# Kernel tuning notes

Hardware: AMD Instinct MI355X
Metric: run time of the kernel (lower is better)

Reference implementation:

```python
import jax, jax.numpy as jnp
import numpy as np

DIM = 1024
AUX = 3
B, S = 32, 1024
ENC_D = DIM * AUX  # 3072


def setup_inputs() -> dict:
    key = jax.random.key(0)
    ks = jax.random.split(key, 5)
    sc1 = 1.0 / np.sqrt(DIM * (AUX + 1))
    sc3 = 1.0 / np.sqrt(ENC_D)
    return {
        "hidden_state": jax.random.normal(ks[0], (B, DIM), jnp.float32),
        "encoder_outputs": jax.random.normal(ks[1], (B, S, ENC_D), jnp.float32),
        "W1": jax.random.normal(ks[2], (DIM, DIM * (AUX + 1)), jnp.float32) * sc1,
        "b1": jnp.zeros((DIM,), jnp.float32),
        "w2": jax.random.normal(ks[3], (1, DIM), jnp.float32) * (1.0 / np.sqrt(DIM)),
        "W3": jax.random.normal(ks[4], (DIM, ENC_D), jnp.float32) * sc3,
        "b3": jnp.zeros((DIM,), jnp.float32),
    }


def reference(hidden_state, encoder_outputs, W1, b1, w2, W3, b3):
    # hidden_state: (B, dim); encoder_outputs: (B, S, dim*aux)
    Bsz, Slen, _ = encoder_outputs.shape
    h = jnp.broadcast_to(hidden_state[:, None, :], (Bsz, Slen, hidden_state.shape[-1]))
    inputs = jnp.concatenate([encoder_outputs, h], axis=2)  # (B, S, dim*(aux+1))
    # score MLP: tanh(linear1) -> linear2 (no bias)
    hidden = jnp.tanh(jnp.einsum('bsf,df->bsd', inputs, W1) + b1)  # (B, S, dim)
    e = jnp.einsum('bsd,od->bso', hidden, w2)[..., 0]  # (B, S)
    alpha = jax.nn.softmax(e, axis=1)
    context = jnp.einsum('bs,bsf->bf', alpha, encoder_outputs)  # (B, dim*aux)
    return jnp.einsum('bf,df->bd', context, W3) + b3  # (B, dim)
```

## Files before the change

### kernel.cpp

```cpp
#include <hip/hip_runtime.h>
#include <hip/hip_bf16.h>


typedef float          fx4 __attribute__((ext_vector_type(4)));
typedef short          sv8 __attribute__((ext_vector_type(8)));
typedef unsigned short uv4 __attribute__((ext_vector_type(4)));
typedef unsigned int   ui4 __attribute__((ext_vector_type(4)));

__device__ __forceinline__ unsigned short f2bf(float x) {
  unsigned u = __float_as_uint(x);
  return (unsigned short)((u + 0x7FFFu + ((u >> 16) & 1u)) >> 16);
}

__device__ __forceinline__ unsigned cvtpk(float lo, float hi) {
  unsigned r;
  asm("v_cvt_pk_bf16_f32 %0, %1, %2" : "=v"(r) : "v"(lo), "v"(hi));
  return r;
}
__device__ __forceinline__ ui4 pack8(fx4 a, fx4 b) {
  ui4 v;
  v[0] = cvtpk(a[0], a[1]); v[1] = cvtpk(a[2], a[3]);
  v[2] = cvtpk(b[0], b[1]); v[3] = cvtpk(b[2], b[3]);
  return v;
}

__global__ void convw1_kernel(const float* __restrict__ W1, unsigned short* __restrict__ W1a) {
  int id = blockIdx.x * 256 + threadIdx.x;
  int d = id / 768, fi = id - d * 768;
  fx4 v = ((const fx4*)W1)[d * 1024 + fi];
  uv4 r; r[0] = f2bf(v[0]); r[1] = f2bf(v[1]); r[2] = f2bf(v[2]); r[3] = f2bf(v[3]);
  ((uv4*)W1a)[d * 768 + fi] = r;
}

__global__ void hbias_kernel(const float* __restrict__ hs, const float* __restrict__ W1,
                             const float* __restrict__ b1, float* __restrict__ hb) {
  int idx = (blockIdx.x << 2) + (threadIdx.x >> 6);
  int lane = threadIdx.x & 63;
  int b = idx >> 10, d = idx & 1023;
  const fx4* hv = (const fx4*)hs;
  const fx4* wv = (const fx4*)W1;
  float s = 0.f;
#pragma unroll
  for (int i = 0; i < 4; ++i) {
    int k4 = lane + (i << 6);
    fx4 h = hv[(b << 8) + k4];
    fx4 w = wv[d * 1024 + 768 + k4];
    s += h[0] * w[0] + h[1] * w[1] + h[2] * w[2] + h[3] * w[3];
  }
#pragma unroll
  for (int off = 32; off; off >>= 1) s += __shfl_xor(s, off);
  if (lane == 0) hb[idx] = s + b1[d];
}

__global__ __launch_bounds__(512, 2)
void gemm_score(const float* __restrict__ enc,
                const unsigned short* __restrict__ W1a,
                const float* __restrict__ hb,
                const float* __restrict__ w2,
                float* __restrict__ pe) {
  __shared__ __align__(16) unsigned short As[2][8192];
  __shared__ __align__(16) unsigned short Bs[2][8192];

  const int t = threadIdx.x;
  const int lane = t & 63, wid = t >> 6;
  const int wm = wid >> 2, wn = wid & 3;

  const int bid = blockIdx.x;
  const int lg = ((bid & 7) << 6) | (bid >> 3);
  const int mt = lg >> 2, nt = lg & 3;
  const int row0 = mt << 8;
  const int col0 = nt << 8;

  const fx4* encv = (const fx4*)enc;

  const int ar = t >> 1, ah = t & 1;
  const int agb = (row0 + ar) * 768 + ah * 4;
  const int awb = ar * 32;
  const int ws0 = ((2 * ah + 0) ^ (ar & 3)) << 3;
  const int ws1 = ((2 * ah + 1) ^ (ar & 3)) << 3;

  const unsigned short* bsrc0 =
      W1a + (col0 + 32 * wid + (lane >> 2)) * 3072 + (((lane & 3) ^ ((lane >> 2) & 3)) << 3);
  const unsigned short* bsrc1 = bsrc0 + 16 * 3072;
  const int bdst0 = (32 * wid) * 32;
  const int bdst1 = (32 * wid + 16) * 32;

  const int r15 = lane & 15, q = lane >> 4;
  const int offA = (wm * 128 + r15) * 32 + ((q ^ (r15 & 3)) << 3);
  const int offB = (wn * 64 + r15) * 32 + ((q ^ (r15 & 3)) << 3);

  fx4 acc[8][4] = {};
  fx4 pa[4];

#define A_LOAD(kt)                                                    \
  { _Pragma("unroll")                                                 \
    for (int j = 0; j < 4; ++j) pa[j] = encv[agb + (kt) * 8 + j]; }
#define A_WRITE(bq)                                                   \
  { *(ui4*)&As[bq][awb + ws0] = pack8(pa[0], pa[1]);                  \
    *(ui4*)&As[bq][awb + ws1] = pack8(pa[2], pa[3]); }
#define B_ISSUE(bq, kt)                                               \
  { __builtin_amdgcn_global_load_lds(                                 \
        (const __attribute__((address_space(1))) void*)(bsrc0 + (kt) * 32), \
        (__attribute__((address_space(3))) void*)&Bs[bq][bdst0], 16, 0, 0); \
    __builtin_amdgcn_global_load_lds(                                 \
        (const __attribute__((address_space(1))) void*)(bsrc1 + (kt) * 32), \
        (__attribute__((address_space(3))) void*)&Bs[bq][bdst1], 16, 0, 0); }
#define COMPUTE(p)                                                    \
  { sv8 af[8], bfv[4];                                                \
    _Pragma("unroll")                                                 \
    for (int mi = 0; mi < 8; ++mi) af[mi] = *(const sv8*)&As[p][offA + mi * 512]; \
    _Pragma("unroll")                                                 \
    for (int ni = 0; ni < 4; ++ni) bfv[ni] = *(const sv8*)&Bs[p][offB + ni * 512]; \
    __builtin_amdgcn_s_setprio(1);                                    \
    _Pragma("unroll")                                                 \
    for (int mi = 0; mi < 8; ++mi)                                    \
      _Pragma("unroll")                                               \
      for (int ni = 0; ni < 4; ++ni)                                  \
        acc[mi][ni] = __builtin_amdgcn_mfma_f32_16x16x32_bf16(af[mi], bfv[ni], acc[mi][ni], 0, 0, 0); \
    __builtin_amdgcn_s_setprio(0); }
#define ITER(kt, p)                                                   \
  { COMPUTE(p)                                                        \
    if ((kt) < 95) { A_WRITE(p ^ 1) }                                 \
    if ((kt) < 94) { A_LOAD((kt) + 2) }                               \
    asm volatile("s_waitcnt lgkmcnt(0)" ::: "memory");                \
    __builtin_amdgcn_s_barrier();                                     \
    __builtin_amdgcn_sched_barrier(0);                                \
    if ((kt) < 94) {                                                  \
      B_ISSUE(p, (kt) + 2)                                            \
      asm volatile("s_waitcnt vmcnt(6)" ::: "memory");                \
    } else if ((kt) == 94) {                                          \
      asm volatile("s_waitcnt vmcnt(0)" ::: "memory");                \
    }                                                                 \
    __builtin_amdgcn_s_barrier(); }

  A_LOAD(0)
  B_ISSUE(0, 0)
  A_WRITE(0)
  A_LOAD(1)
  B_ISSUE(1, 1)
  asm volatile("s_waitcnt lgkmcnt(0)" ::: "memory");
  asm volatile("s_waitcnt vmcnt(6)" ::: "memory");
  __builtin_amdgcn_s_barrier();

  for (int kt2 = 0; kt2 < 48; ++kt2) {
    const int kt = kt2 * 2;
    ITER(kt, 0)
    ITER(kt + 1, 1)
  }

  const int b = row0 >> 10;
  float w2v[4], hbv[4];
#pragma unroll
  for (int ni = 0; ni < 4; ++ni) {
    int c = col0 + wn * 64 + ni * 16 + r15;
    w2v[ni] = w2[c];
    hbv[ni] = hb[(b << 10) + c];
  }
#pragma unroll
  for (int mi = 0; mi < 8; ++mi) {
#pragma unroll
    for (int j = 0; j < 4; ++j) {
      float pz = 0.f;
#pragma unroll
      for (int ni = 0; ni < 4; ++ni)
        pz += tanhf(acc[mi][ni][j] + hbv[ni]) * w2v[ni];
      pz += __shfl_xor(pz, 1); pz += __shfl_xor(pz, 2);
      pz += __shfl_xor(pz, 4); pz += __shfl_xor(pz, 8);
      if (r15 == 0) {
        int row = row0 + wm * 128 + mi * 16 + (q << 2) + j;
        pe[(row << 4) + (nt << 2) + wn] = pz;
      }
    }
  }
#undef A_LOAD
#undef A_WRITE
#undef B_ISSUE
#undef COMPUTE
#undef ITER
}

__global__ void softmax_kernel(const float* __restrict__ pe, float* __restrict__ alpha) {
  int b = blockIdx.x, t = threadIdx.x;
  int lane = t & 63, wid = t >> 6;
  float ev[4];
#pragma unroll
  for (int r = 0; r < 4; ++r) {
    int s = t + r * 256;
    const float* p = pe + ((b << 10) + s) * 16;
    float sum = 0.f;
#pragma unroll
    for (int i = 0; i < 16; ++i) sum += p[i];
    ev[r] = sum;
  }
  float m = fmaxf(fmaxf(ev[0], ev[1]), fmaxf(ev[2], ev[3]));
#pragma unroll
  for (int off = 32; off; off >>= 1) m = fmaxf(m, __shfl_xor(m, off));
  __shared__ float red[8];
  if (lane == 0) red[wid] = m;
  __syncthreads();
  m = fmaxf(fmaxf(red[0], red[1]), fmaxf(red[2], red[3]));
  float p4[4], ls = 0.f;
#pragma unroll
  for (int r = 0; r < 4; ++r) { p4[r] = expf(ev[r] - m); ls += p4[r]; }
#pragma unroll
  for (int off = 32; off; off >>= 1) ls += __shfl_xor(ls, off);
  if (lane == 0) red[4 + wid] = ls;
  __syncthreads();
  float inv = 1.0f / (red[4] + red[5] + red[6] + red[7]);
#pragma unroll
  for (int r = 0; r < 4; ++r) alpha[(b << 10) + t + r * 256] = p4[r] * inv;
}

__global__ void ctxpart_kernel(const float* __restrict__ enc, const float* __restrict__ alpha,
                               float* __restrict__ part) {
  int bid = blockIdx.x, b = bid >> 4, sc = bid & 15;
  int t = threadIdx.x;
  __shared__ float sal[64];
  if (t < 64) sal[t] = alpha[(b << 10) + (sc << 6) + t];
  __syncthreads();
  const fx4* ev = (const fx4*)enc;
  fx4 a0 = {}, a1 = {}, a2 = {};
  int base = ((b << 10) + (sc << 6)) * 768;
  for (int si = 0; si < 64; ++si) {
    float a = sal[si];
    const fx4* rp = ev + base + si * 768;
    a0 += a * rp[t];
    a1 += a * rp[256 + t];
    a2 += a * rp[512 + t];
  }
  fx4* pp = (fx4*)part;
  int pb = ((b << 4) + sc) * 768;
  pp[pb + t] = a0; pp[pb + 256 + t] = a1; pp[pb + 512 + t] = a2;
}

__global__ void ctxreduce_kernel(const float* __restrict__ part, float* __restrict__ ctx) {
  int j = blockIdx.x * 256 + threadIdx.x;
  int b = j / 768, fi = j - b * 768;
  const fx4* pp = (const fx4*)part;
  fx4 s = {};
#pragma unroll
  for (int i = 0; i < 16; ++i) s += pp[((b << 4) + i) * 768 + fi];
  ((fx4*)ctx)[b * 768 + fi] = s;
}

__global__ void final_kernel(const float* __restrict__ ctx, const float* __restrict__ W3,
                             const float* __restrict__ b3, float* __restrict__ out) {
  int idx = (blockIdx.x << 2) + (threadIdx.x >> 6);
  int lane = threadIdx.x & 63;
  int b = idx >> 10, d = idx & 1023;
  const fx4* cv = (const fx4*)ctx;
  const fx4* wv = (const fx4*)W3;
  float s = 0.f;
#pragma unroll
  for (int i = 0; i < 12; ++i) {
    int f4 = lane + (i << 6);
    fx4 c = cv[b * 768 + f4];
    fx4 w = wv[d * 768 + f4];
    s += c[0] * w[0] + c[1] * w[1] + c[2] * w[2] + c[3] * w[3];
  }
#pragma unroll
  for (int off = 32; off; off >>= 1) s += __shfl_xor(s, off);
  if (lane == 0) out[idx] = s + b3[d];
}

extern "C" void kernel_launch(void* const* d_in, const int* in_sizes, int n_in,
                              void* d_out, int out_size, void* d_ws, size_t ws_size,
                              hipStream_t stream) {
  const float* hs  = (const float*)d_in[0];
  const float* enc = (const float*)d_in[1];
  const float* W1  = (const float*)d_in[2];
  const float* b1  = (const float*)d_in[3];
  const float* w2  = (const float*)d_in[4];
  const float* W3  = (const float*)d_in[5];
  const float* b3  = (const float*)d_in[6];
  float* out = (float*)d_out;

  char* ws = (char*)d_ws;
  unsigned short* W1a = (unsigned short*)(ws);
  float* pe    = (float*)(ws + 6291456);
  float* alpha = (float*)(ws + 8388608);
  float* hb    = (float*)(ws + 8519680);
  float* ctx   = (float*)(ws + 8650752);
  float* part  = (float*)(ws + 9043968);

  convw1_kernel<<<3072, 256, 0, stream>>>(W1, W1a);
  hbias_kernel<<<8192, 256, 0, stream>>>(hs, W1, b1, hb);
  gemm_score<<<512, 512, 0, stream>>>(enc, W1a, hb, w2, pe);
  softmax_kernel<<<32, 256, 0, stream>>>(pe, alpha);
  ctxpart_kernel<<<512, 256, 0, stream>>>(enc, alpha, part);
  ctxreduce_kernel<<<96, 256, 0, stream>>>(part, ctx);
  final_kernel<<<8192, 256, 0, stream>>>(ctx, W3, b3, out);
}
```

Baseline: 412.7 us.

## Shrink score GEMM tile to 128x128 with 4 waves and more blocks

Re-tiles the score GEMM from 256x256 tiles with 8 waves per block to 128x128 tiles with 4 waves, launching 2048 blocks instead of 512, with occupancy target raised to 3 blocks per CU. LDS buffers and per-wave accumulators are halved, and the tile-to-block swizzle and partial-score indexing are adjusted to the 8 column tiles. The setprio hints and sched_barrier are dropped and the lgkmcnt wait moves after the B issue. This is meant to give more blocks per CU and better latency hiding, but smaller tiles halve operand reuse, so global and L2 traffic for both enc and W1 roughly doubles.

```diff
diff --git a/kernel.cpp b/kernel.cpp
--- a/kernel.cpp
+++ b/kernel.cpp
@@ -52,52 +52,50 @@
   if (lane == 0) hb[idx] = s + b1[d];
 }
 
-__global__ __launch_bounds__(512, 2)
+__global__ __launch_bounds__(256, 3)
 void gemm_score(const float* __restrict__ enc,
                 const unsigned short* __restrict__ W1a,
                 const float* __restrict__ hb,
                 const float* __restrict__ w2,
                 float* __restrict__ pe) {
-  __shared__ __align__(16) unsigned short As[2][8192];
-  __shared__ __align__(16) unsigned short Bs[2][8192];
+  __shared__ __align__(16) unsigned short As[2][4096];
+  __shared__ __align__(16) unsigned short Bs[2][4096];
 
   const int t = threadIdx.x;
   const int lane = t & 63, wid = t >> 6;
-  const int wm = wid >> 2, wn = wid & 3;
+  const int wm = wid >> 1, wn = wid & 1;
 
   const int bid = blockIdx.x;
-  const int lg = ((bid & 7) << 6) | (bid >> 3);
-  const int mt = lg >> 2, nt = lg & 3;
-  const int row0 = mt << 8;
-  const int col0 = nt << 8;
+  const int lg = ((bid & 7) << 8) | (bid >> 3);
+  const int mt = lg >> 3, ntile = lg & 7;
+  const int row0 = mt << 7;
+  const int col0 = ntile << 7;
 
   const fx4* encv = (const fx4*)enc;
 
   const int ar = t >> 1, ah = t & 1;
   const int agb = (row0 + ar) * 768 + ah * 4;
   const int awb = ar * 32;
-  const int ws0 = ((2 * ah + 0) ^ (ar & 3)) << 3;
-  const int ws1 = ((2 * ah + 1) ^ (ar & 3)) << 3;
-
-  const unsigned short* bsrc0 =
-      W1a + (col0 + 32 * wid + (lane >> 2)) * 3072 + (((lane & 3) ^ ((lane >> 2) & 3)) << 3);
-  const unsigned short* bsrc1 = bsrc0 + 16 * 3072;
-  const int bdst0 = (32 * wid) * 32;
-  const int bdst1 = (32 * wid + 16) * 32;
-
-  const int r15 = lane & 15, q = lane >> 4;
-  const int offA = (wm * 128 + r15) * 32 + ((q ^ (r15 & 3)) << 3);
-  const int offB = (wn * 64 + r15) * 32 + ((q ^ (r15 & 3)) << 3);
-
-  fx4 acc[8][4] = {};
+  const int ws0 = (((ah << 1) + 0) ^ (ar & 3)) << 3;
+  const int ws1 = (((ah << 1) + 1) ^ (ar & 3)) << 3;
+
+  const int bcl = (wid << 4) + (lane >> 2);
+  const int bsw = (((lane & 3) ^ ((lane >> 2) & 3)) << 3);
+  const unsigned short* bsrc0 = W1a + (col0 + bcl) * 3072 + bsw;
+  const unsigned short* bsrc1 = W1a + (col0 + 64 + bcl) * 3072 + bsw;
+  const int bdst0 = bcl << 5;
+  const int bdst1 = (64 + bcl) << 5;
+
+  const int r15 = lane & 15, qv = lane >> 4;
+  const int offA = (wm * 64 + r15) * 32 + ((qv ^ (r15 & 3)) << 3);
+  const int offB = (wn * 64 + r15) * 32 + ((qv ^ (r15 & 3)) << 3);
+
+  fx4 acc[4][4] = {};
   fx4 pa[4];
 
-#define A_LOAD(kt)                                                    \
-  { _Pragma("unroll")                                                 \
-    for (int j = 0; j < 4; ++j) pa[j] = encv[agb + (kt) * 8 + j]; }
-#define A_WRITE(bq)                                                   \
-  { *(ui4*)&As[bq][awb + ws0] = pack8(pa[0], pa[1]);                  \
-    *(ui4*)&As[bq][awb + ws1] = pack8(pa[2], pa[3]); }
+#define A_LOAD(kt) { _Pragma("unroll") for (int j = 0; j < 4; ++j) pa[j] = encv[agb + (kt) * 8 + j]; }
+#define A_WRITE(bq) { *(ui4*)&As[bq][awb + ws0] = pack8(pa[0], pa[1]); \
+                      *(ui4*)&As[bq][awb + ws1] = pack8(pa[2], pa[3]); }
 #define B_ISSUE(bq, kt)                                               \
   { __builtin_amdgcn_global_load_lds(                                 \
         (const __attribute__((address_space(1))) void*)(bsrc0 + (kt) * 32), \
@@ -106,31 +104,28 @@
         (const __attribute__((address_space(1))) void*)(bsrc1 + (kt) * 32), \
         (__attribute__((address_space(3))) void*)&Bs[bq][bdst1], 16, 0, 0); }
 #define COMPUTE(p)                                                    \
-  { sv8 af[8], bfv[4];                                                \
+  { sv8 af[4], bfv[4];                                                \
     _Pragma("unroll")                                                 \
-    for (int mi = 0; mi < 8; ++mi) af[mi] = *(const sv8*)&As[p][offA + mi * 512]; \
+    for (int mi = 0; mi < 4; ++mi) af[mi] = *(const sv8*)&As[p][offA + mi * 512]; \
     _Pragma("unroll")                                                 \
     for (int ni = 0; ni < 4; ++ni) bfv[ni] = *(const sv8*)&Bs[p][offB + ni * 512]; \
-    __builtin_amdgcn_s_setprio(1);                                    \
     _Pragma("unroll")                                                 \
-    for (int mi = 0; mi < 8; ++mi)                                    \
+    for (int mi = 0; mi < 4; ++mi)                                    \
       _Pragma("unroll")                                               \
       for (int ni = 0; ni < 4; ++ni)                                  \
-        acc[mi][ni] = __builtin_amdgcn_mfma_f32_16x16x32_bf16(af[mi], bfv[ni], acc[mi][ni], 0, 0, 0); \
-    __builtin_amdgcn_s_setprio(0); }
+        acc[mi][ni] = __builtin_amdgcn_mfma_f32_16x16x32_bf16(af[mi], bfv[ni], acc[mi][ni], 0, 0, 0); }
 #define ITER(kt, p)                                                   \
   { COMPUTE(p)                                                        \
-    if ((kt) < 95) { A_WRITE(p ^ 1) }                                 \
+    if ((kt) < 95) { A_WRITE(p ^ 1) }       \
     if ((kt) < 94) { A_LOAD((kt) + 2) }                               \
-    asm volatile("s_waitcnt lgkmcnt(0)" ::: "memory");                \
-    __builtin_amdgcn_s_barrier();                                     \
-    __builtin_amdgcn_sched_barrier(0);                                \
+    __builtin_amdgcn_s_barrier();            \
     if ((kt) < 94) {                                                  \
       B_ISSUE(p, (kt) + 2)                                            \
       asm volatile("s_waitcnt vmcnt(6)" ::: "memory");                \
     } else if ((kt) == 94) {                                          \
       asm volatile("s_waitcnt vmcnt(0)" ::: "memory");                \
     }                                                                 \
+    asm volatile("s_waitcnt lgkmcnt(0)" ::: "memory");                \
     __builtin_amdgcn_s_barrier(); }
 
   A_LOAD(0)
@@ -138,8 +133,8 @@
   A_WRITE(0)
   A_LOAD(1)
   B_ISSUE(1, 1)
+  asm volatile("s_waitcnt vmcnt(6)" ::: "memory");
   asm volatile("s_waitcnt lgkmcnt(0)" ::: "memory");
-  asm volatile("s_waitcnt vmcnt(6)" ::: "memory");
   __builtin_amdgcn_s_barrier();
 
   for (int kt2 = 0; kt2 < 48; ++kt2) {
@@ -157,7 +152,7 @@
     hbv[ni] = hb[(b << 10) + c];
   }
 #pragma unroll
-  for (int mi = 0; mi < 8; ++mi) {
+  for (int mi = 0; mi < 4; ++mi) {
 #pragma unroll
     for (int j = 0; j < 4; ++j) {
       float pz = 0.f;
@@ -167,8 +162,8 @@
       pz += __shfl_xor(pz, 1); pz += __shfl_xor(pz, 2);
       pz += __shfl_xor(pz, 4); pz += __shfl_xor(pz, 8);
       if (r15 == 0) {
-        int row = row0 + wm * 128 + mi * 16 + (q << 2) + j;
-        pe[(row << 4) + (nt << 2) + wn] = pz;
+        int row = row0 + wm * 64 + mi * 16 + (qv << 2) + j;
+        pe[(row << 4) + (ntile << 1) + wn] = pz;
       }
     }
   }
@@ -285,7 +280,7 @@
 
   convw1_kernel<<<3072, 256, 0, stream>>>(W1, W1a);
   hbias_kernel<<<8192, 256, 0, stream>>>(hs, W1, b1, hb);
-  gemm_score<<<512, 512, 0, stream>>>(enc, W1a, hb, w2, pe);
+  gemm_score<<<2048, 256, 0, stream>>>(enc, W1a, hb, w2, pe);
   softmax_kernel<<<32, 256, 0, stream>>>(pe, alpha);
   ctxpart_kernel<<<512, 256, 0, stream>>>(enc, alpha, part);
   ctxreduce_kernel<<<96, 256, 0, stream>>>(part, ctx);
```

Measured after the change: 500.4 us. 1.21x slower.

## Deepen A prefetch to two register stages and rework LDS padding and swizzle

Applied to the files above, without the earlier changes.

The encoder-tile global loads now run three k-steps ahead, using two register staging buffers, so global latency is better hidden behind the MFMA loop. The A tile in shared memory switches from an XOR swizzle to a padded row stride of 40, and the B tile gets a new 64-wide XOR swizzle to cut LDS bank conflicts on fragment reads. The s_setprio hints and a sched_barrier are removed, and the LDS waitcnt moves after the B issue. In exchange the kernel uses more registers and more shared memory, which could lower occupancy at two blocks per CU.

```diff
diff --git a/kernel.cpp b/kernel.cpp
--- a/kernel.cpp
+++ b/kernel.cpp
@@ -58,7 +58,7 @@
                 const float* __restrict__ hb,
                 const float* __restrict__ w2,
                 float* __restrict__ pe) {
-  __shared__ __align__(16) unsigned short As[2][8192];
+  __shared__ __align__(16) unsigned short As[2][10240];
   __shared__ __align__(16) unsigned short Bs[2][8192];
 
   const int t = threadIdx.x;
@@ -67,79 +67,75 @@
 
   const int bid = blockIdx.x;
   const int lg = ((bid & 7) << 6) | (bid >> 3);
-  const int mt = lg >> 2, nt = lg & 3;
+  const int mt = lg >> 2, ntile = lg & 3;
   const int row0 = mt << 8;
-  const int col0 = nt << 8;
+  const int col0 = ntile << 8;
 
   const fx4* encv = (const fx4*)enc;
 
   const int ar = t >> 1, ah = t & 1;
   const int agb = (row0 + ar) * 768 + ah * 4;
-  const int awb = ar * 32;
-  const int ws0 = ((2 * ah + 0) ^ (ar & 3)) << 3;
-  const int ws1 = ((2 * ah + 1) ^ (ar & 3)) << 3;
-
+  const int awb = ar * 40 + ah * 16;
+
+  const int l3 = lane >> 3, l7 = lane & 7;
+  const int pre = l7 ^ l3;
   const unsigned short* bsrc0 =
-      W1a + (col0 + 32 * wid + (lane >> 2)) * 3072 + (((lane & 3) ^ ((lane >> 2) & 3)) << 3);
-  const unsigned short* bsrc1 = bsrc0 + 16 * 3072;
-  const int bdst0 = (32 * wid) * 32;
-  const int bdst1 = (32 * wid + 16) * 32;
-
-  const int r15 = lane & 15, q = lane >> 4;
-  const int offA = (wm * 128 + r15) * 32 + ((q ^ (r15 & 3)) << 3);
-  const int offB = (wn * 64 + r15) * 32 + ((q ^ (r15 & 3)) << 3);
+      W1a + (size_t)(col0 + wid * 32 + 2 * l3 + (pre >> 2)) * 3072 + (pre & 3) * 8;
+  const unsigned short* bsrc1 = bsrc0 + (size_t)16 * 3072;
+  const int bdst0 = (wid * 16) * 64;
+  const int bdst1 = (wid * 16 + 8) * 64;
+
+  const int r15 = lane & 15, qv = lane >> 4;
+  const int aro = (wm * 128 + r15) * 40 + qv * 8;
+  const int cb = wn * 64 + r15;
+  const int bro = (cb >> 1) * 64 + (((((cb & 1) << 2) + qv) ^ ((cb >> 1) & 7)) << 3);
 
   fx4 acc[8][4] = {};
-  fx4 pa[4];
-
-#define A_LOAD(kt)                                                    \
-  { _Pragma("unroll")                                                 \
-    for (int j = 0; j < 4; ++j) pa[j] = encv[agb + (kt) * 8 + j]; }
-#define A_WRITE(bq)                                                   \
-  { *(ui4*)&As[bq][awb + ws0] = pack8(pa[0], pa[1]);                  \
-    *(ui4*)&As[bq][awb + ws1] = pack8(pa[2], pa[3]); }
-#define B_ISSUE(bq, kt)                                               \
+  fx4 pa[2][4];
+
+#define A_LOAD(s, kt) { _Pragma("unroll") for (int j = 0; j < 4; ++j) pa[s][j] = encv[agb + (kt) * 8 + j]; }
+#define A_WRITE(s, buf) { *(ui4*)&As[buf][awb] = pack8(pa[s][0], pa[s][1]); \
+                          *(ui4*)&As[buf][awb + 8] = pack8(pa[s][2], pa[s][3]); }
+#define B_ISSUE(buf, kt)                                              \
   { __builtin_amdgcn_global_load_lds(                                 \
         (const __attribute__((address_space(1))) void*)(bsrc0 + (kt) * 32), \
-        (__attribute__((address_space(3))) void*)&Bs[bq][bdst0], 16, 0, 0); \
+        (__attribute__((address_space(3))) void*)&Bs[buf][bdst0], 16, 0, 0); \
     __builtin_amdgcn_global_load_lds(                                 \
         (const __attribute__((address_space(1))) void*)(bsrc1 + (kt) * 32), \
-        (__attribute__((address_space(3))) void*)&Bs[bq][bdst1], 16, 0, 0); }
+        (__attribute__((address_space(3))) void*)&Bs[buf][bdst1], 16, 0, 0); }
 #define COMPUTE(p)                                                    \
   { sv8 af[8], bfv[4];                                                \
     _Pragma("unroll")                                                 \
-    for (int mi = 0; mi < 8; ++mi) af[mi] = *(const sv8*)&As[p][offA + mi * 512]; \
+    for (int mi = 0; mi < 8; ++mi) af[mi] = *(const sv8*)&As[p][aro + mi * 640]; \
     _Pragma("unroll")                                                 \
-    for (int ni = 0; ni < 4; ++ni) bfv[ni] = *(const sv8*)&Bs[p][offB + ni * 512]; \
-    __builtin_amdgcn_s_setprio(1);                                    \
+    for (int ni = 0; ni < 4; ++ni) bfv[ni] = *(const sv8*)&Bs[p][bro + ni * 512]; \
     _Pragma("unroll")                                                 \
     for (int mi = 0; mi < 8; ++mi)                                    \
       _Pragma("unroll")                                               \
       for (int ni = 0; ni < 4; ++ni)                                  \
-        acc[mi][ni] = __builtin_amdgcn_mfma_f32_16x16x32_bf16(af[mi], bfv[ni], acc[mi][ni], 0, 0, 0); \
-    __builtin_amdgcn_s_setprio(0); }
+        acc[mi][ni] = __builtin_amdgcn_mfma_f32_16x16x32_bf16(af[mi], bfv[ni], acc[mi][ni], 0, 0, 0); }
 #define ITER(kt, p)                                                   \
   { COMPUTE(p)                                                        \
-    if ((kt) < 95) { A_WRITE(p ^ 1) }                                 \
-    if ((kt) < 94) { A_LOAD((kt) + 2) }                               \
-    asm volatile("s_waitcnt lgkmcnt(0)" ::: "memory");                \
-    __builtin_amdgcn_s_barrier();                                     \
-    __builtin_amdgcn_sched_barrier(0);                                \
+    if ((kt) < 95) { A_WRITE(p ^ 1, p ^ 1) }    \
+    if ((kt) < 93) { A_LOAD(p ^ 1, (kt) + 3) }   \
+    __builtin_amdgcn_s_barrier();                \
     if ((kt) < 94) {                                                  \
       B_ISSUE(p, (kt) + 2)                                            \
       asm volatile("s_waitcnt vmcnt(6)" ::: "memory");                \
     } else if ((kt) == 94) {                                          \
       asm volatile("s_waitcnt vmcnt(0)" ::: "memory");                \
     }                                                                 \
+    asm volatile("s_waitcnt lgkmcnt(0)" ::: "memory");                \
     __builtin_amdgcn_s_barrier(); }
 
-  A_LOAD(0)
+  A_LOAD(0, 0)
+  A_LOAD(1, 1)
   B_ISSUE(0, 0)
-  A_WRITE(0)
-  A_LOAD(1)
+  A_WRITE(0, 0)
   B_ISSUE(1, 1)
+  A_LOAD(0, 2)
+  asm volatile("s_waitcnt vmcnt(6)" ::: "memory");
   asm volatile("s_waitcnt lgkmcnt(0)" ::: "memory");
-  asm volatile("s_waitcnt vmcnt(6)" ::: "memory");
   __builtin_amdgcn_s_barrier();
 
   for (int kt2 = 0; kt2 < 48; ++kt2) {
@@ -167,8 +163,8 @@
       pz += __shfl_xor(pz, 1); pz += __shfl_xor(pz, 2);
       pz += __shfl_xor(pz, 4); pz += __shfl_xor(pz, 8);
       if (r15 == 0) {
-        int row = row0 + wm * 128 + mi * 16 + (q << 2) + j;
-        pe[(row << 4) + (nt << 2) + wn] = pz;
+        int row = row0 + wm * 128 + mi * 16 + (qv << 2) + j;
+        pe[(row << 4) + (ntile << 2) + wn] = pz;
       }
     }
   }
```

New measurement: 415.7 us. No clear change (+0.7%).
